# Kernel tuning notes

Measured on AMD Instinct MI355X. Metric: run time of the kernel, lower is better.

The kernel has to match this reference:

```python
import jax, jax.numpy as jnp
import numpy as np

WIN = 20  # rebalancing window length, hard-coded as 20 in the source


def setup_inputs() -> dict:
    key = jax.random.key(0)
    kY = jax.random.fold_in(key, 1)
    # returns-like data, small scale so covariances are well behaved
    Y = jax.random.normal(kY, (20000, 256), dtype=jnp.float32) * 0.01
    a = jnp.ones((1,), dtype=jnp.float32)
    b = jnp.ones((1,), dtype=jnp.float32)
    return {"Y": Y, "a": a, "b": b, "lag": 24}


def _ewma_gmv(Y, a, lag):
    n, p = Y.shape
    nt = lag * WIN                      # train window length = 480
    n_win = n // WIN - lag              # number of backtest windows

    starts = jnp.arange(n_win) * WIN                      # (i-lag)*20
    tr_idx = starts[:, None] + jnp.arange(nt)             # [n_win, nt]
    te_idx = (starts + nt)[:, None] + jnp.arange(WIN)
    Y_tr = Y[tr_idx]                                      # [W, nt, p]
    Y_te = Y[te_idx]

    # EWMA weights: w_t = a**(nt-1-t), normalized to sum to nt (shared by all windows)
    t = jnp.arange(nt - 1, -1, -1, dtype=Y.dtype)
    w = a[0] ** t
    w = w / w.sum() * nt                                  # [nt]

    # EWMA mean and centered data
    mean = jnp.einsum('t,wtp->wp', w, Y_tr) / nt          # [W, p]
    Yc = Y_tr - mean[:, None, :]                          # [W, nt, p]

    # EWMA sample covariance ('S' estimator):
    # Sigma = Yc^T diag(w) Yc / nt / (1 - sum(w^2)/nt^2)
    denom = nt * (1.0 - (w ** 2).sum() / (nt * nt))
    Sigma = jnp.einsum('wtp,wtq->wpq', Yc * w[None, :, None], Yc) / denom

    # GMV portfolio: w_opt = Sigma^{-1} wb / (wb^T Sigma^{-1} wb), wb = 1/p
    wb = jnp.full((p,), 1.0 / p, dtype=Y.dtype)
    x = jnp.linalg.solve(Sigma, jnp.broadcast_to(wb, (n_win, p))[..., None])[..., 0]
    w_opt = x / jnp.einsum('wp,p->w', x, wb)[:, None]     # [W, p]

    # realized test-window portfolio returns
    r = jnp.einsum('wtp,wp->wt', Y_te, w_opt)
    res_e = r.sum(axis=1)                                 # realized return over window
    res_s = jnp.var(r, axis=1, ddof=1)                    # realized daily variance

    vol = jnp.sqrt(res_s.mean() * 252.0)
    mu = res_e.mean() / WIN * 252.0
    sharpe = mu / vol
    return vol, mu, sharpe


def reference(Y, a, b, lag):
    # b only enters alpha/beta, which are unused by the 'S' estimator branch
    return _ewma_gmv(Y, a, lag)
```

## Files before the change

kernel.cpp:

```cpp
#include <hip/hip_runtime.h>
#include <math.h>

#define N_TOT   20000
#define P       256
#define WIN     20
#define LAG     24
#define NT      (LAG*WIN)
#define NB      (N_TOT/WIN)
#define NW      (NB - LAG)
#define N16T    136
#define TILEB   (N16T*256)
#define DTE     TILEB
#define NSUB4   (N16T*16)
#define ODW     (TILEB/4)
#define CG_ITERS 12

#if defined(__has_builtin)
# if __has_builtin(__builtin_amdgcn_cvt_pk_f32_fp8) && __has_builtin(__builtin_amdgcn_cvt_pk_fp8_f32)
#  define HW_FP8 1
# endif
#endif
#ifndef HW_FP8
# define HW_FP8 0
#endif

typedef float v2f   __attribute__((ext_vector_type(2)));
typedef float f32x4 __attribute__((ext_vector_type(4)));

__device__ __forceinline__ float bfr2f(unsigned short s) {
    union { unsigned int u; float f; } z; z.u = ((unsigned int)s) << 16; return z.f;
}
__device__ __forceinline__ float lo16f(unsigned int u) {
    union { unsigned int u; float f; } z; z.u = u << 16; return z.f;
}
__device__ __forceinline__ float hi16f(unsigned int u) {
    union { unsigned int u; float f; } z; z.u = u & 0xffff0000u; return z.f;
}
__device__ __forceinline__ unsigned short f2bfr(float f) {
    union { unsigned int u; float f; } z; z.f = f;
    unsigned int u = z.u;
    unsigned int r = (u + 0x7fffu + ((u >> 16) & 1u)) >> 16;
    return (unsigned short)r;
}

__device__ __forceinline__ unsigned char f2fp8(float f) {
#if HW_FP8
    int r = __builtin_amdgcn_cvt_pk_fp8_f32(f, f, 0, false);
    return (unsigned char)(r & 0xff);
#else
    union { float f; unsigned int u; } z; z.f = f;
    unsigned int s = (z.u >> 24) & 0x80u;
    float af = fabsf(f);
    if (af < 0.0009765625f) return (unsigned char)s;
    if (af >= 448.f)        return (unsigned char)(s | 0x7Eu);
    if (af < 0.015625f) {
        unsigned int m = (unsigned int)(af * 512.f + 0.5f);
        return (unsigned char)(s | m);
    }
    unsigned int au = (z.u & 0x7fffffffu) + 0x00080000u;
    unsigned int e  = (au >> 23) - 120u;
    unsigned int m  = (au >> 20) & 0x7u;
    if (e >= 16u) return (unsigned char)(s | 0x7Eu);
    return (unsigned char)(s | (e << 3) | m);
#endif
}

#if !HW_FP8
__device__ __forceinline__ float fp82f(unsigned char b) {
    unsigned int e = (b >> 3) & 0xFu;
    unsigned int m = b & 7u;
    float v;
    if (e) { union { unsigned int u; float f; } t; t.u = ((e + 120u) << 23) | (m << 20); v = t.f; }
    else   { v = (float)m * 0.001953125f; }
    return (b & 0x80u) ? -v : v;
}
#endif

__device__ __forceinline__ unsigned int pack4_fp8(float a, float b, float c, float d) {
#if HW_FP8
    int u = __builtin_amdgcn_cvt_pk_fp8_f32(a, b, 0, false);
    u = __builtin_amdgcn_cvt_pk_fp8_f32(c, d, u, true);
    return (unsigned int)u;
#else
    return (unsigned int)f2fp8(a) | ((unsigned int)f2fp8(b) << 8) |
           ((unsigned int)f2fp8(c) << 16) | ((unsigned int)f2fp8(d) << 24);
#endif
}
__device__ __forceinline__ void unpack4_fp8(unsigned int u, float* o) {
#if HW_FP8
    v2f lo = __builtin_amdgcn_cvt_pk_f32_fp8(u, false);
    v2f hi = __builtin_amdgcn_cvt_pk_f32_fp8(u, true);
    o[0] = lo.x; o[1] = lo.y; o[2] = hi.x; o[3] = hi.y;
#else
    o[0] = fp82f((unsigned char)(u & 0xff));
    o[1] = fp82f((unsigned char)((u >> 8) & 0xff));
    o[2] = fp82f((unsigned char)((u >> 16) & 0xff));
    o[3] = fp82f((unsigned char)((u >> 24) & 0xff));
#endif
}

__device__ __forceinline__ f32x4 mfma_fp8(long a, long b, f32x4 c) {
    return __builtin_amdgcn_mfma_f32_16x16x32_fp8_fp8(a, b, c, 0, 0, 0);
}

__device__ __forceinline__ unsigned int vperm(unsigned int s0, unsigned int s1,
                                              unsigned int sel) {
    unsigned int d;
    asm("v_perm_b32 %0, %1, %2, %3" : "=v"(d) : "v"(s0), "v"(s1), "v"(sel));
    return d;
}

__global__ void k_fallback(float* out) { out[0] = 0.f; out[1] = 0.f; out[2] = 0.f; }

__global__ __launch_bounds__(256)
void k_blocks(const float* __restrict__ Y, const float* __restrict__ pa,
              unsigned short* __restrict__ D, float* __restrict__ Dd,
              float* __restrict__ R, int base_blk)
{
    __shared__ float Ys[WIN][P];
    __shared__ float Yw[WIN][P];
    const int krel = blockIdx.x;
    const int kg   = base_blk + krel;
    const int tid  = threadIdx.x;
    const float a  = pa[0];

    float wts[WIN];
    wts[WIN-1] = 1.f;
    #pragma unroll
    for (int t = WIN-2; t >= 0; --t) wts[t] = wts[t+1] * a;

    float racc = 0.f;
    #pragma unroll
    for (int t = 0; t < WIN; ++t) {
        float v  = Y[(size_t)(kg*WIN + t)*P + tid];
        float wv = wts[t] * v;
        Ys[t][tid] = v;
        Yw[t][tid] = wv;
        racc += wv;
    }
    R[(size_t)kg*P + tid] = racc;
    __syncthreads();

    unsigned short* Dk = D + (size_t)krel * DTE;
    for (int T = tid; T < NSUB4; T += 256) {
        int t16 = T >> 4, sub = T & 15;
        int ti = (int)((sqrtf(8.f*(float)t16 + 1.f) - 1.f) * 0.5f);
        while ((ti+1)*(ti+2)/2 <= t16) ++ti;
        while (ti*(ti+1)/2 > t16) --ti;
        int tj = t16 - ti*(ti+1)/2;
        int r4 = sub >> 2, c4 = sub & 3;
        int i0 = ti*16 + r4*4, j0 = tj*16 + c4*4;

        float c[4][4] = {{0.f}};
        for (int t = 0; t < WIN; ++t) {
            float4 av = *(const float4*)&Yw[t][i0];
            float4 bv = *(const float4*)&Ys[t][j0];
            float aa[4] = {av.x, av.y, av.z, av.w};
            float bb[4] = {bv.x, bv.y, bv.z, bv.w};
            #pragma unroll
            for (int r = 0; r < 4; ++r)
                #pragma unroll
                for (int cc = 0; cc < 4; ++cc)
                    c[r][cc] = fmaf(aa[r], bb[cc], c[r][cc]);
        }
        unsigned short* tp = Dk + (size_t)t16*256 + (r4*4)*16 + c4*4;
        #pragma unroll
        for (int r = 0; r < 4; ++r) {
            unsigned int u0 = (unsigned int)f2bfr(c[r][0]) | ((unsigned int)f2bfr(c[r][1]) << 16);
            unsigned int u1 = (unsigned int)f2bfr(c[r][2]) | ((unsigned int)f2bfr(c[r][3]) << 16);
            uint2 uv; uv.x = u0; uv.y = u1;
            *(uint2*)(tp + r*16) = uv;
        }
        if (i0 == j0) {
            #pragma unroll
            for (int r = 0; r < 4; ++r)
                Dd[(size_t)krel*P + i0 + r] = c[r][r];
        }
    }
}

__global__ __launch_bounds__(256)
void k_scale(const float* __restrict__ Dd, const float* __restrict__ R,
             const float* __restrict__ pa, float* __restrict__ Sc,
             float* __restrict__ Sscale, float* __restrict__ acc, int base_w)
{
    __shared__ float kred[4];
    const int wl  = blockIdx.x;
    const int w   = base_w + wl;
    const int i   = threadIdx.x;
    const int lane = i & 63;
    const int wid  = i >> 6;
    const float a = pa[0];

    if (base_w == 0 && wl == 0 && i == 0) { acc[0] = 0.f; acc[1] = 0.f; }

    float a20 = 1.f;
    #pragma unroll
    for (int q = 0; q < WIN; ++q) a20 *= a;
    float Wsum;
    if (fabsf(a - 1.f) < 1e-6f) Wsum = (float)NT;
    else {
        float a480 = 1.f;
        #pragma unroll
        for (int q = 0; q < LAG; ++q) a480 *= a20;
        Wsum = (a480 - 1.f) / (a - 1.f);
    }
    const float invW = 1.f / Wsum;

    float s = 0.f, sd = 0.f, tp = 1.f;
    for (int b = LAG-1; b >= 0; --b) {
        s  = fmaf(tp, R [(size_t)(w  + b)*P + i], s);
        sd = fmaf(tp, Dd[(size_t)(wl + b)*P + i], sd);
        tp *= a20;
    }
    Sc[(size_t)wl*P + i] = s * sqrtf(invW);

    float d_i = sd - s*s*invW;
    float dm = d_i;
    #pragma unroll
    for (int off = 32; off; off >>= 1) dm = fmaxf(dm, __shfl_down(dm, off));
    if (lane == 0) kred[wid] = dm;
    __syncthreads();
    if (i == 0) {
        float maxd = fmaxf(fmaxf(kred[0], kred[1]), fmaxf(kred[2], kred[3]));
        Sscale[wl] = 64.f / maxd;
    }
}

__global__ __launch_bounds__(256)
void k_conv(const unsigned short* __restrict__ D, const float* __restrict__ pa,
            const float* __restrict__ Sc, const float* __restrict__ Sscale,
            unsigned char* __restrict__ Mt, int SC_)
{
    const int od = blockIdx.x*256 + threadIdx.x;
    const int w0 = blockIdx.y * SC_;
    const float a = pa[0];

    float a20 = 1.f;
    #pragma unroll
    for (int q = 0; q < WIN; ++q) a20 *= a;
    float c23 = 1.f;
    #pragma unroll
    for (int q = 0; q < LAG-1; ++q) c23 *= a20;
    const float nc23 = -c23;

    const int t = od >> 6, q = od & 63;
    int ti = (int)((sqrtf(8.f*(float)t + 1.f) - 1.f) * 0.5f);
    while ((ti+1)*(ti+2)/2 <= t) ++ti;
    while (ti*(ti+1)/2 > t) --ti;
    const int tj = t - ti*(ti+1)/2;
    const int i  = ti*16 + (q >> 2);
    const int j0 = tj*16 + (q & 3)*4;

    const unsigned short* Dp = D + (size_t)w0*DTE + od*4;

    float m0 = 0.f, m1 = 0.f, m2 = 0.f, m3 = 0.f;
    unsigned int rg0[LAG], rg1[LAG];
    #pragma unroll
    for (int b = 0; b < LAG; ++b) {
        uint2 ev = *(const uint2*)(Dp + (size_t)b*DTE);
        rg0[b] = ev.x; rg1[b] = ev.y;
        m0 = fmaf(m0, a20, lo16f(ev.x));
        m1 = fmaf(m1, a20, hi16f(ev.x));
        m2 = fmaf(m2, a20, lo16f(ev.y));
        m3 = fmaf(m3, a20, hi16f(ev.y));
    }

    for (int sg = 0; sg < SC_; sg += LAG) {
        #pragma unroll
        for (int k = 0; k < LAG; ++k) {
            const int s = sg + k;
            if (s >= SC_) break;
            const int w = w0 + s;
            const float* scr = Sc + (size_t)w*P;
            float  sci = scr[i];
            float4 scj = *(const float4*)(scr + j0);
            float  ssc = Sscale[w];
            float c0 = fmaf(-sci, scj.x, m0) * ssc;
            float c1 = fmaf(-sci, scj.y, m1) * ssc;
            float c2 = fmaf(-sci, scj.z, m2) * ssc;
            float c3 = fmaf(-sci, scj.w, m3) * ssc;
            *(unsigned int*)(Mt + (size_t)w*TILEB + od*4) = pack4_fp8(c0, c1, c2, c3);
            uint2 ev = *(const uint2*)(Dp + (size_t)(s + LAG)*DTE);
            m0 = fmaf(fmaf(nc23, lo16f(rg0[k]), m0), a20, lo16f(ev.x));
            m1 = fmaf(fmaf(nc23, hi16f(rg0[k]), m1), a20, hi16f(ev.x));
            m2 = fmaf(fmaf(nc23, lo16f(rg1[k]), m2), a20, lo16f(ev.y));
            m3 = fmaf(fmaf(nc23, hi16f(rg1[k]), m3), a20, hi16f(ev.y));
            rg0[k] = ev.x; rg1[k] = ev.y;
        }
    }
}

__global__ __launch_bounds__(512, 4)
void k_solve(const unsigned char* __restrict__ Mt, const float* __restrict__ Y,
             float* __restrict__ acc, int base_w)
{
    __shared__ __align__(16) unsigned char Ms[TILEB];
    __shared__ __align__(16) float xs[P];
    __shared__ __align__(16) unsigned int rf8[128];
    __shared__ __align__(16) float red[32];
    __shared__ float qs[WIN];

    const int wloc = blockIdx.x;
    const int w    = base_w + wloc;
    const int tid  = threadIdx.x;
    const int lane = tid & 63;
    const int wid  = tid >> 6;
    const int g    = lane >> 4;
    const int r15  = lane & 15;

    {
        const unsigned char* src = Mt + (size_t)wloc * TILEB;
        typedef const __attribute__((address_space(1))) unsigned int* gp1;
        typedef __attribute__((address_space(3))) unsigned int* lp3;
        for (int cb = wid; cb < 34; cb += 8) {
            __builtin_amdgcn_global_load_lds((gp1)(src + cb*1024 + lane*16),
                                             (lp3)(Ms + cb*1024), 16, 0, 0);
        }
    }
    if (tid < 64)       rf8[tid] = 0x38383838u;
    else if (tid < 128) rf8[tid] = 0u;

    const float* Yte = Y + (size_t)(w*WIN + NT) * P;
    float4 ypre0 = *(const float4*)&Yte[(size_t)(wid     )*P + lane*4];
    float4 ypre1 = *(const float4*)&Yte[(size_t)(wid + 8 )*P + lane*4];
    float4 ypre2 = make_float4(0.f, 0.f, 0.f, 0.f);
    if (wid < 4) ypre2 = *(const float4*)&Yte[(size_t)(wid + 16)*P + lane*4];

    __syncthreads();

    const int RTa[2] = { wid, 15 - wid };
    const unsigned int selk  = (unsigned int)(r15 & 3) * 0x0101u + 0x0400u;
    const unsigned int sel2  = 0x05040100u;
    long afr[2][8];
    #pragma unroll
    for (int t = 0; t < 2; ++t) {
        const int rt = RTa[t];
        #pragma unroll
        for (int ks = 0; ks < 8; ++ks) {
            const int kt = ks*2 + (g >> 1);
            const int sb = (g & 1) * 8;
            long v;
            if (kt <= rt) {
                v = *(const long*)&Ms[(size_t)(rt*(rt+1)/2 + kt)*256 + r15*16 + sb];
            } else {
                const unsigned char* tp2 =
                    &Ms[(size_t)(kt*(kt+1)/2 + rt)*256 + sb*16 + (r15 & ~3)];
                unsigned int a0 = *(const unsigned int*)(tp2 +  0);
                unsigned int a1 = *(const unsigned int*)(tp2 + 16);
                unsigned int a2 = *(const unsigned int*)(tp2 + 32);
                unsigned int a3 = *(const unsigned int*)(tp2 + 48);
                unsigned int e0 = *(const unsigned int*)(tp2 + 64);
                unsigned int e1 = *(const unsigned int*)(tp2 + 80);
                unsigned int e2 = *(const unsigned int*)(tp2 + 96);
                unsigned int e3 = *(const unsigned int*)(tp2 + 112);
                unsigned int b0 = vperm(vperm(a3, a2, selk), vperm(a1, a0, selk), sel2);
                unsigned int b1 = vperm(vperm(e3, e2, selk), vperm(e1, e0, selk), sel2);
                v = (long)(((unsigned long)b1 << 32) | b0);
            }
            afr[t][ks] = v;
        }
    }

    float rr[2][4], pp[2][4], ssv[2][4], xx[2][4];
    #pragma unroll
    for (int t = 0; t < 2; ++t)
        #pragma unroll
        for (int r = 0; r < 4; ++r) { rr[t][r] = 1.f; pp[t][r] = 0.f; ssv[t][r] = 0.f; xx[t][r] = 0.f; }

    const unsigned char* rfb = (const unsigned char*)rf8;
    const unsigned char* rbh = rfb + (g << 6);
    float mu_p = 1.f, alpha_p = 1.f;
    for (int it = 0; it < CG_ITERS; ++it) {
        f32x4 ah0 = {0.f,0.f,0.f,0.f}, ah1 = {0.f,0.f,0.f,0.f};
        f32x4 al0 = {0.f,0.f,0.f,0.f}, al1 = {0.f,0.f,0.f,0.f};
        #pragma unroll
        for (int kp = 0; kp < 4; ++kp) {
            long2 bh = *(const long2*)(rbh + kp*16);
            long2 bl = *(const long2*)(rbh + 256 + kp*16);
            ah0 = mfma_fp8(afr[0][2*kp],   bh.x, ah0);
            ah1 = mfma_fp8(afr[1][2*kp],   bh.x, ah1);
            al0 = mfma_fp8(afr[0][2*kp],   bl.x, al0);
            al1 = mfma_fp8(afr[1][2*kp],   bl.x, al1);
            ah0 = mfma_fp8(afr[0][2*kp+1], bh.y, ah0);
            ah1 = mfma_fp8(afr[1][2*kp+1], bh.y, ah1);
            al0 = mfma_fp8(afr[0][2*kp+1], bl.y, al0);
            al1 = mfma_fp8(afr[1][2*kp+1], bl.y, al1);
        }
        float w0[4], w1[4];
        #pragma unroll
        for (int r = 0; r < 4; ++r) {
            w0[r] = fmaf(al0[r], 0.0625f, ah0[r]);
            w1[r] = fmaf(al1[r], 0.0625f, ah1[r]);
        }

        float mu_c = 0.f, nu_c = 0.f;
        #pragma unroll
        for (int r = 0; r < 4; ++r) {
            mu_c += rr[0][r]*rr[0][r] + rr[1][r]*rr[1][r];
            nu_c  = fmaf(rr[0][r], w0[r], nu_c);
            nu_c  = fmaf(rr[1][r], w1[r], nu_c);
        }
        if (r15 != 0) { mu_c = 0.f; nu_c = 0.f; }
        mu_c += __shfl_down(mu_c, 32); nu_c += __shfl_down(nu_c, 32);
        mu_c += __shfl_down(mu_c, 16); nu_c += __shfl_down(nu_c, 16);
        if (lane == 0) *(float2*)&red[wid*2] = make_float2(mu_c, nu_c);
        __syncthreads();
        float4 q0 = *(const float4*)&red[0];
        float4 q1 = *(const float4*)&red[4];
        float4 q2 = *(const float4*)&red[8];
        float4 q3 = *(const float4*)&red[12];
        float mu = q0.x + q0.z + q1.x + q1.z + q2.x + q2.z + q3.x + q3.z;
        float nu = q0.y + q0.w + q1.y + q1.w + q2.y + q2.w + q3.y + q3.w;

        float beta  = (it == 0) ? 0.f : mu / mu_p;
        float alpha = (it == 0) ? mu / nu
                                : mu / (nu - beta * mu / alpha_p);
        mu_p = mu; alpha_p = alpha;

        #pragma unroll
        for (int t = 0; t < 2; ++t)
            #pragma unroll
            for (int r = 0; r < 4; ++r) {
                float wv = t ? w1[r] : w0[r];
                pp[t][r]  = fmaf(beta, pp[t][r], rr[t][r]);
                ssv[t][r] = fmaf(beta, ssv[t][r], wv);
                xx[t][r]  = fmaf(alpha, pp[t][r], xx[t][r]);
                rr[t][r]  = fmaf(-alpha, ssv[t][r], rr[t][r]);
            }

        if (r15 == 0 && it != CG_ITERS-1) {
            #pragma unroll
            for (int t = 0; t < 2; ++t) {
                unsigned int hv = pack4_fp8(rr[t][0], rr[t][1], rr[t][2], rr[t][3]);
                float dec[4];
                unpack4_fp8(hv, dec);
                unsigned int lv = pack4_fp8((rr[t][0]-dec[0])*16.f, (rr[t][1]-dec[1])*16.f,
                                            (rr[t][2]-dec[2])*16.f, (rr[t][3]-dec[3])*16.f);
                int gk  = (RTa[t]*2 + (g >> 1)) & 3;
                int idx = gk*16 + (RTa[t] >> 1)*2 + (g & 1);
                rf8[idx]      = hv;
                rf8[64 + idx] = lv;
            }
        }
        __syncthreads();
    }

    if (r15 == 0) {
        #pragma unroll
        for (int t = 0; t < 2; ++t)
            *(float4*)&xs[RTa[t]*16 + g*4] =
                make_float4(xx[t][0], xx[t][1], xx[t][2], xx[t][3]);
    }
    float sv = 0.f;
    #pragma unroll
    for (int t = 0; t < 2; ++t)
        #pragma unroll
        for (int r = 0; r < 4; ++r) sv += xx[t][r];
    if (r15 != 0) sv = 0.f;
    sv += __shfl_down(sv, 32); sv += __shfl_down(sv, 16);
    if (lane == 0) red[wid] = sv;
    __syncthreads();
    float sumx = red[0]+red[1]+red[2]+red[3]+red[4]+red[5]+red[6]+red[7];

    {
        float4 xv = *(const float4*)&xs[lane*4];
        float q;
        q = ypre0.x*xv.x + ypre0.y*xv.y + ypre0.z*xv.z + ypre0.w*xv.w;
        #pragma unroll
        for (int off = 32; off; off >>= 1) q += __shfl_down(q, off);
        if (lane == 0) qs[wid] = q;
        q = ypre1.x*xv.x + ypre1.y*xv.y + ypre1.z*xv.z + ypre1.w*xv.w;
        #pragma unroll
        for (int off = 32; off; off >>= 1) q += __shfl_down(q, off);
        if (lane == 0) qs[wid + 8] = q;
        if (wid < 4) {
            q = ypre2.x*xv.x + ypre2.y*xv.y + ypre2.z*xv.z + ypre2.w*xv.w;
            #pragma unroll
            for (int off = 32; off; off >>= 1) q += __shfl_down(q, off);
            if (lane == 0) qs[wid + 16] = q;
        }
    }
    __syncthreads();

    if (tid == 0) {
        float scl = (float)P / sumx;
        float rsv[WIN];
        float re = 0.f;
        #pragma unroll
        for (int t = 0; t < WIN; ++t) { rsv[t] = qs[t]*scl; re += rsv[t]; }
        float mean = re / (float)WIN;
        float var = 0.f;
        #pragma unroll
        for (int t = 0; t < WIN; ++t) { float d = rsv[t] - mean; var = fmaf(d, d, var); }
        var /= (float)(WIN - 1);
        atomicAdd(&acc[0], re);
        atomicAdd(&acc[1], var);
    }
}

__global__ void k_final(const float* __restrict__ acc, float* __restrict__ out)
{
    float mean_s = acc[1] / (float)NW;
    float vol = sqrtf(mean_s * 252.f);
    float mu  = (acc[0] / (float)NW) / (float)WIN * 252.f;
    out[0] = vol;
    out[1] = mu;
    out[2] = mu / vol;
}

static inline size_t align_up(size_t x) { return (x + 255) & ~(size_t)255; }

extern "C" void kernel_launch(void* const* d_in, const int* in_sizes, int n_in,
                              void* d_out, int out_size, void* d_ws, size_t ws_size,
                              hipStream_t stream)
{
    const float* Y  = (const float*)d_in[0];
    const float* pa = (const float*)d_in[1];
    float* out = (float*)d_out;

    static const int nch_opts[] = {1, 2, 4, 8, 16, 61};
    int CW = -1;
    size_t oDd = 0, oMt = 0, oR = 0, oSc = 0, oSs = 0, oAcc = 0;
    for (int oi = 0; oi < 6; ++oi) {
        int cw = NW / nch_opts[oi];
        size_t dB  = align_up((size_t)(cw + LAG) * DTE * 2);
        size_t ddB = align_up((size_t)(cw + LAG) * P * 4);
        size_t mB  = align_up((size_t)cw * TILEB);
        size_t rB  = align_up((size_t)NB * P * 4);
        size_t scB = align_up((size_t)cw * P * 4);
        size_t ssB = align_up((size_t)cw * 4);
        size_t tot = dB + ddB + mB + rB + scB + ssB + 256;
        if (tot <= ws_size) {
            CW = cw; oDd = dB; oMt = dB + ddB; oR = oMt + mB;
            oSc = oR + rB; oSs = oSc + scB; oAcc = oSs + ssB;
            break;
        }
    }
    if (CW < 0) {
        hipLaunchKernelGGL(k_fallback, dim3(1), dim3(1), 0, stream, out);
        return;
    }
    const int NCH  = NW / CW;
    const int SC   = (CW % 61 == 0) ? 61 : CW;
    const int NSUB = CW / SC;

    char* ws = (char*)d_ws;
    unsigned short* D   = (unsigned short*)(ws);
    float*          Dd  = (float*)(ws + oDd);
    unsigned char*  Mt  = (unsigned char*)(ws + oMt);
    float*          R   = (float*)(ws + oR);
    float*          Sc  = (float*)(ws + oSc);
    float*          Ssc = (float*)(ws + oSs);
    float*          acc = (float*)(ws + oAcc);

    for (int c = 0; c < NCH; ++c) {
        const int base_w = c * CW;
        hipLaunchKernelGGL(k_blocks, dim3(CW + LAG),      dim3(256), 0, stream,
                           Y, pa, D, Dd, R, base_w);
        hipLaunchKernelGGL(k_scale,  dim3(CW),            dim3(256), 0, stream,
                           Dd, R, pa, Sc, Ssc, acc, base_w);
        hipLaunchKernelGGL(k_conv,   dim3(ODW/256, NSUB), dim3(256), 0, stream,
                           D, pa, Sc, Ssc, Mt, SC);
        hipLaunchKernelGGL(k_solve,  dim3(CW),            dim3(512), 0, stream,
                           Mt, Y, acc, base_w);
    }
    hipLaunchKernelGGL(k_final, dim3(1), dim3(1), 0, stream, acc, out);
}
```

Baseline: 197.8 us.

## Widen per-thread covariance micro-tile to 4x8 and stagger block starts with sleep

The per-block outer-product kernel now gives each thread a 4x8 register tile instead of 4x4. This halves the work items per 16x16 tile and reuses each Yw load across twice as many FMAs, with wider 16-byte stores of bf16 results, while the diagonal extraction is adjusted for the new shape. Separately, the solve kernel inserts s_sleep delays keyed on window index bits, staggering block start times, presumably to reduce memory contention. The sleep adds latency and the larger tile raises register pressure.

```diff
diff --git a/kernel.cpp b/kernel.cpp
--- a/kernel.cpp
+++ b/kernel.cpp
@@ -11,7 +11,7 @@
 #define N16T    136
 #define TILEB   (N16T*256)
 #define DTE     TILEB
-#define NSUB4   (N16T*16)
+#define NU48    (N16T*8)
 #define ODW     (TILEB/4)
 #define CG_ITERS 12
 
@@ -142,39 +142,42 @@
     __syncthreads();
 
     unsigned short* Dk = D + (size_t)krel * DTE;
-    for (int T = tid; T < NSUB4; T += 256) {
-        int t16 = T >> 4, sub = T & 15;
+    for (int U = tid; U < NU48; U += 256) {
+        int t16 = U >> 3, u = U & 7;
         int ti = (int)((sqrtf(8.f*(float)t16 + 1.f) - 1.f) * 0.5f);
         while ((ti+1)*(ti+2)/2 <= t16) ++ti;
         while (ti*(ti+1)/2 > t16) --ti;
         int tj = t16 - ti*(ti+1)/2;
-        int r4 = sub >> 2, c4 = sub & 3;
-        int i0 = ti*16 + r4*4, j0 = tj*16 + c4*4;
-
-        float c[4][4] = {{0.f}};
+        int r4 = u >> 1, c8 = u & 1;
+        int i0 = ti*16 + r4*4, j0 = tj*16 + c8*8;
+
+        float c[4][8] = {{0.f}};
         for (int t = 0; t < WIN; ++t) {
             float4 av = *(const float4*)&Yw[t][i0];
-            float4 bv = *(const float4*)&Ys[t][j0];
+            float4 b0 = *(const float4*)&Ys[t][j0];
+            float4 b1 = *(const float4*)&Ys[t][j0+4];
             float aa[4] = {av.x, av.y, av.z, av.w};
-            float bb[4] = {bv.x, bv.y, bv.z, bv.w};
+            float bb[8] = {b0.x, b0.y, b0.z, b0.w, b1.x, b1.y, b1.z, b1.w};
             #pragma unroll
             for (int r = 0; r < 4; ++r)
                 #pragma unroll
-                for (int cc = 0; cc < 4; ++cc)
+                for (int cc = 0; cc < 8; ++cc)
                     c[r][cc] = fmaf(aa[r], bb[cc], c[r][cc]);
         }
-        unsigned short* tp = Dk + (size_t)t16*256 + (r4*4)*16 + c4*4;
+        unsigned short* tp = Dk + (size_t)t16*256 + (r4*4)*16 + c8*8;
         #pragma unroll
         for (int r = 0; r < 4; ++r) {
-            unsigned int u0 = (unsigned int)f2bfr(c[r][0]) | ((unsigned int)f2bfr(c[r][1]) << 16);
-            unsigned int u1 = (unsigned int)f2bfr(c[r][2]) | ((unsigned int)f2bfr(c[r][3]) << 16);
-            uint2 uv; uv.x = u0; uv.y = u1;
-            *(uint2*)(tp + r*16) = uv;
-        }
-        if (i0 == j0) {
+            uint4 uv;
+            uv.x = (unsigned int)f2bfr(c[r][0]) | ((unsigned int)f2bfr(c[r][1]) << 16);
+            uv.y = (unsigned int)f2bfr(c[r][2]) | ((unsigned int)f2bfr(c[r][3]) << 16);
+            uv.z = (unsigned int)f2bfr(c[r][4]) | ((unsigned int)f2bfr(c[r][5]) << 16);
+            uv.w = (unsigned int)f2bfr(c[r][6]) | ((unsigned int)f2bfr(c[r][7]) << 16);
+            *(uint4*)(tp + r*16) = uv;
+        }
+        if (ti == tj && (r4 >> 1) == c8) {
             #pragma unroll
             for (int r = 0; r < 4; ++r)
-                Dd[(size_t)krel*P + i0 + r] = c[r][r];
+                Dd[(size_t)krel*P + i0 + r] = c[r][r4*4 + r - c8*8];
         }
     }
 }
@@ -326,6 +329,11 @@
     float4 ypre1 = *(const float4*)&Yte[(size_t)(wid + 8 )*P + lane*4];
     float4 ypre2 = make_float4(0.f, 0.f, 0.f, 0.f);
     if (wid < 4) ypre2 = *(const float4*)&Yte[(size_t)(wid + 16)*P + lane*4];
+
+    {
+        const int skey = (wloc >> 8) & 3;
+        for (int sk = 0; sk < skey; ++sk) __builtin_amdgcn_s_sleep(42);
+    }
 
     __syncthreads();
 
```

Result: slower. 494.8 us (+150.2%).
